# Kernel tuning notes

Measured on AMD Instinct MI355X. Metric: run time of the kernel, lower is better.

Reference implementation:

```python
import jax, jax.numpy as jnp
import numpy as np
import math

HIDDEN, N_HEADS = 128, 4
HEAD_DIM = HIDDEN // N_HEADS

def _silu(x):
    return x * jax.nn.sigmoid(x)

def _ln(x, g, b, eps=1e-5):
    m = jnp.mean(x, axis=-1, keepdims=True)
    v = jnp.mean((x - m) ** 2, axis=-1, keepdims=True)
    return (x - m) / jnp.sqrt(v + eps) * g + b


def setup_inputs() -> dict:
    key = jax.random.key(0)
    B, N, ND, ED, HD = 2, 512, 64, 32, 128
    ks = iter(jax.random.split(key, 64))
    def p(*shape):
        return jax.random.normal(next(ks), shape, jnp.float32) * 0.05
    d = {}
    d['h'] = jax.random.normal(next(ks), (B, N, ND), jnp.float32)
    d['x'] = jax.random.normal(next(ks), (B, N, 2), jnp.float32)
    d['e'] = jax.random.normal(next(ks), (B, N, N, ED), jnp.float32)
    msg_in = 2 * ND + ED + 1  # 161
    d['msg_W1'] = p(msg_in, HD); d['msg_b1'] = jnp.zeros((HD,), jnp.float32)
    d['msg_ln_g'] = jnp.ones((HD,), jnp.float32); d['msg_ln_b'] = jnp.zeros((HD,), jnp.float32)
    d['msg_W2'] = p(HD, HD); d['msg_b2'] = jnp.zeros((HD,), jnp.float32)
    d['msg_W3'] = p(HD, HD); d['msg_b3'] = jnp.zeros((HD,), jnp.float32)
    d['attn_W1'] = p(HD, HD // 2); d['attn_b1'] = jnp.zeros((HD // 2,), jnp.float32)
    d['attn_W2'] = p(HD // 2, N_HEADS); d['attn_b2'] = jnp.zeros((N_HEADS,), jnp.float32)
    d['val_W'] = p(HD, HD); d['val_b'] = jnp.zeros((HD,), jnp.float32)
    d['coord_W1'] = p(HD, HD // 2); d['coord_b1'] = jnp.zeros((HD // 2,), jnp.float32)
    d['coord_W2'] = p(HD // 2, 1)  # bias=False
    d['node_W1'] = p(ND + HD, HD); d['node_b1'] = jnp.zeros((HD,), jnp.float32)
    d['node_ln_g'] = jnp.ones((HD,), jnp.float32); d['node_ln_b'] = jnp.zeros((HD,), jnp.float32)
    d['node_W2'] = p(HD, ND); d['node_b2'] = jnp.zeros((ND,), jnp.float32)
    d['edge_W1'] = p(ED + HD, HD); d['edge_b1'] = jnp.zeros((HD,), jnp.float32)
    d['edge_ln_g'] = jnp.ones((HD,), jnp.float32); d['edge_ln_b'] = jnp.zeros((HD,), jnp.float32)
    d['edge_W2'] = p(HD, ED); d['edge_b2'] = jnp.zeros((ED,), jnp.float32)
    d['nn_g'] = jnp.ones((ND,), jnp.float32); d['nn_b'] = jnp.zeros((ND,), jnp.float32)
    d['en_g'] = jnp.ones((ED,), jnp.float32); d['en_b'] = jnp.zeros((ED,), jnp.float32)
    d['coord_scale'] = jnp.float32(0.1)
    return d


def reference(h, x, e,
              msg_W1, msg_b1, msg_ln_g, msg_ln_b, msg_W2, msg_b2, msg_W3, msg_b3,
              attn_W1, attn_b1, attn_W2, attn_b2, val_W, val_b,
              coord_W1, coord_b1, coord_W2,
              node_W1, node_b1, node_ln_g, node_ln_b, node_W2, node_b2,
              edge_W1, edge_b1, edge_ln_g, edge_ln_b, edge_W2, edge_b2,
              nn_g, nn_b, en_g, en_b, coord_scale):
    B, N, ND = h.shape
    # pairwise geometry: x_diff[b,i,j] = x[b,j] - x[b,i]
    x_diff = x[:, None, :, :] - x[:, :, None, :]           # (B,N,N,2)
    distances = jnp.linalg.norm(x_diff, axis=-1, keepdims=True)  # (B,N,N,1)
    h_i = jnp.broadcast_to(h[:, :, None, :], (B, N, N, ND))
    h_j = jnp.broadcast_to(h[:, None, :, :], (B, N, N, ND))
    msg_input = jnp.concatenate([h_i, h_j, e, distances], axis=-1)
    # message MLP (dropout is identity in eval)
    m = _silu(msg_input @ msg_W1 + msg_b1)
    m = _ln(m, msg_ln_g, msg_ln_b)
    m = _silu(m @ msg_W2 + msg_b2)
    messages = m @ msg_W3 + msg_b3                          # (B,N,N,HIDDEN)
    # attention over j (axis=2), multi-head
    attn_logits = (_silu(messages @ attn_W1 + attn_b1) @ attn_W2 + attn_b2)
    attn_logits = attn_logits / math.sqrt(HEAD_DIM)
    attn_weights = jax.nn.softmax(attn_logits, axis=2)      # (B,N,N,H)
    values = (messages @ val_W + val_b).reshape(B, N, N, N_HEADS, HEAD_DIM)
    messages_attended = jnp.einsum('bijh,bijhd->bihd', attn_weights, values)
    messages_attended = messages_attended.reshape(B, N, HIDDEN)
    # equivariant coordinate update
    coord_weights = _silu(messages @ coord_W1 + coord_b1) @ coord_W2  # (B,N,N,1)
    coord_weights = jnp.tanh(coord_weights / 10.0)
    x_diff_norm = x_diff / (distances + 1e-8)
    coord_update = jnp.sum(coord_weights * x_diff_norm, axis=2)      # (B,N,2)
    x_new = x + coord_scale * coord_update
    # node update
    h_input = jnp.concatenate([h, messages_attended], axis=-1)
    hh = _silu(h_input @ node_W1 + node_b1)
    hh = _ln(hh, node_ln_g, node_ln_b)
    hh = hh @ node_W2 + node_b2
    h_new = _ln(h + hh, nn_g, nn_b)
    # edge update
    e_input = jnp.concatenate([e, messages], axis=-1)
    ee = _silu(e_input @ edge_W1 + edge_b1)
    ee = _ln(ee, edge_ln_g, edge_ln_b)
    ee = ee @ edge_W2 + edge_b2
    e_new = _ln(e + ee, en_g, en_b)
    return (h_new, x_new, e_new)
```

## Files before the change

kernel.cpp:

```cpp
#include <hip/hip_runtime.h>
#include <math.h>

typedef __attribute__((ext_vector_type(8))) short short8;
typedef __attribute__((ext_vector_type(4))) short short4v;
typedef __attribute__((ext_vector_type(8))) unsigned short u16x8;
typedef __attribute__((ext_vector_type(4))) float f32x4;

#define NN 512
#define JT 32
#define STR 136
#define BUFSZ (JT * STR)
#define E2S 36

#define TOT_W 106496

__device__ __forceinline__ unsigned short f2b(float x) {
    return __builtin_bit_cast(unsigned short, (__bf16)x);
}
__device__ __forceinline__ float b2f(unsigned short v) {
    return __uint_as_float(((unsigned int)v) << 16);
}
__device__ __forceinline__ float silu_f(float v) { return v / (1.f + __expf(-v)); }

__device__ __forceinline__ float half_sum512(float v, float* s_red, int t) {
    if (t < 256) s_red[t] = v;
    __syncthreads();
    int tt = t & 127;
    for (int s = 64; s > 0; s >>= 1) {
        if (t < 256 && tt < s) s_red[t] += s_red[t + s];
        __syncthreads();
    }
    float r = (t < 256) ? s_red[t & 128] : 0.f;
    __syncthreads();
    return r;
}

__device__ __forceinline__ void frag_kf(int loc, int nK, int& k, int& f) {
    int jj = loc & 7;
    int lane = (loc >> 3) & 63;
    int fs = loc >> 9;
    int ks = fs % nK;
    int ft = fs / nK;
    k = ks * 32 + ((lane >> 4) << 3) + jj;
    f = ft * 16 + (lane & 15);
}

extern "C" __global__ void prepack_w(const float* __restrict__ msg_W1, const float* __restrict__ msg_W2,
                                     const float* __restrict__ msg_W3, const float* __restrict__ val_W,
                                     const float* __restrict__ attn_W1, const float* __restrict__ coord_W1,
                                     const float* __restrict__ edge_W1, const float* __restrict__ edge_W2,
                                     unsigned short* __restrict__ ws) {
    int idx = blockIdx.x * 256 + threadIdx.x;
    if (idx >= TOT_W) return;
    float v;
    int k, f;
    if (idx < 16384) {
        frag_kf(idx, 4, k, f);
        v = (k <= 96) ? msg_W1[(64 + k) * 128 + f] : 0.f;
    } else if (idx < 32768) {
        frag_kf(idx - 16384, 4, k, f);
        v = msg_W2[k * 128 + f];
    } else if (idx < 49152) {
        frag_kf(idx - 32768, 4, k, f);
        v = msg_W3[k * 128 + f];
    } else if (idx < 65536) {
        frag_kf(idx - 49152, 4, k, f);
        v = val_W[k * 128 + f];
    } else if (idx < 81920) {
        frag_kf(idx - 65536, 4, k, f);
        v = (f < 64) ? attn_W1[k * 64 + f] : coord_W1[k * 64 + (f - 64)];
    } else if (idx < 102400) {
        frag_kf(idx - 81920, 5, k, f);
        v = (k < 128) ? edge_W1[(32 + k) * 128 + f] : edge_W1[(k - 128) * 128 + f];
    } else {
        frag_kf(idx - 102400, 4, k, f);
        v = edge_W2[k * 32 + f];
    }
    ws[idx] = f2b(v);
}

struct Frag1 { f32x4 a[2]; };

__device__ __forceinline__ short8 wfrag(const unsigned short* base, int nK, int ft, int ks, int lane) {
    return *(const short8*)(base + (((ft * nK + ks) << 9) + (lane << 3)));
}

__device__ __forceinline__ void initF1(Frag1& F, const float* bias, int ft, int lane) {
    int q = lane >> 4;
    f32x4 bv = *(const f32x4*)(bias + ft * 16 + q * 4);
    F.a[0] = bv; F.a[1] = bv;
}

__device__ __forceinline__ void ldb(const unsigned short* B, int kcol, int lane, short8& b0, short8& b1) {
    int q8 = ((lane >> 4) << 3), l15 = lane & 15;
    b0 = *(const short8*)(B + l15 * STR + kcol + q8);
    b1 = *(const short8*)(B + (16 + l15) * STR + kcol + q8);
}

__device__ __forceinline__ void mfma2(Frag1& F, short8 a, short8 b0, short8 b1) {
    F.a[0] = __builtin_amdgcn_mfma_f32_16x16x32_bf16(a, b0, F.a[0], 0, 0, 0);
    F.a[1] = __builtin_amdgcn_mfma_f32_16x16x32_bf16(a, b1, F.a[1], 0, 0, 0);
}

__device__ __forceinline__ void storeF1(const Frag1& F, unsigned short* dbuf, int ft, int lane, int act) {
    int q = lane >> 4, l15 = lane & 15;
#pragma unroll
    for (int ji = 0; ji < 2; ji++) {
        int j = ji * 16 + l15;
        int f0 = ft * 16 + q * 4;
        f32x4 v = F.a[ji];
        short4v p;
#pragma unroll
        for (int r = 0; r < 4; r++) {
            float o = act ? silu_f(v[r]) : v[r];
            p[r] = (short)f2b(o);
        }
        *(short4v*)(dbuf + j * STR + f0) = p;
    }
}

__device__ __forceinline__ void ln_tile(unsigned short* buf, const float* g, const float* bv, int tt) {
    int j = tt >> 3, sub = tt & 7;
    unsigned short* p = buf + j * STR + sub * 16;
    u16x8 r0 = *(u16x8*)p;
    u16x8 r1 = *(u16x8*)(p + 8);
    float v[16];
#pragma unroll
    for (int i = 0; i < 8; i++) { v[i] = b2f(r0[i]); v[8 + i] = b2f(r1[i]); }
    float sm = 0.f;
#pragma unroll
    for (int i = 0; i < 16; i++) sm += v[i];
    sm += __shfl_xor(sm, 1); sm += __shfl_xor(sm, 2); sm += __shfl_xor(sm, 4);
    float mean = sm * 0.0078125f;
    float sq = 0.f;
#pragma unroll
    for (int i = 0; i < 16; i++) { float d = v[i] - mean; sq += d * d; }
    sq += __shfl_xor(sq, 1); sq += __shfl_xor(sq, 2); sq += __shfl_xor(sq, 4);
    float rstd = rsqrtf(sq * 0.0078125f + 1e-5f);
    u16x8 o0, o1;
#pragma unroll
    for (int i = 0; i < 8; i++) {
        o0[i] = f2b((v[i] - mean) * rstd * g[sub * 16 + i] + bv[sub * 16 + i]);
        o1[i] = f2b((v[8 + i] - mean) * rstd * g[sub * 16 + 8 + i] + bv[sub * 16 + 8 + i]);
    }
    *(u16x8*)p = o0;
    *(u16x8*)(p + 8) = o1;
}

extern "C" __global__ __launch_bounds__(512, 4)
void egnn_mfma(const float* __restrict__ h, const float* __restrict__ x, const float* __restrict__ e,
               const float* __restrict__ msg_W1, const float* __restrict__ msg_b1,
               const float* __restrict__ msg_ln_g, const float* __restrict__ msg_ln_b,
               const float* __restrict__ msg_b2, const float* __restrict__ msg_b3,
               const float* __restrict__ attn_b1, const float* __restrict__ attn_W2,
               const float* __restrict__ attn_b2, const float* __restrict__ val_b,
               const float* __restrict__ coord_b1, const float* __restrict__ coord_W2,
               const float* __restrict__ node_W1, const float* __restrict__ node_b1,
               const float* __restrict__ node_ln_g, const float* __restrict__ node_ln_b,
               const float* __restrict__ node_W2, const float* __restrict__ node_b2,
               const float* __restrict__ edge_b1, const float* __restrict__ edge_ln_g,
               const float* __restrict__ edge_ln_b, const float* __restrict__ edge_b2,
               const float* __restrict__ nn_g, const float* __restrict__ nn_b,
               const float* __restrict__ en_g, const float* __restrict__ en_b,
               const float* __restrict__ coord_scale_p,
               const unsigned short* __restrict__ wpk,
               float* __restrict__ out_h, float* __restrict__ out_x, float* __restrict__ out_e) {
    const int t = threadIdx.x;
    const int wave = t >> 6, lane = t & 63;
    const int biA = blockIdx.x * 2;
    const int biB = biA + 1;
    const int b = biA >> 9;

    __shared__ __align__(16) unsigned short smA[3 * BUFSZ];
    __shared__ __align__(16) unsigned short smB[3 * BUFSZ];
    unsigned short* B0a = smA;
    unsigned short* B1a = smA + BUFSZ;
    unsigned short* B2a = smA + 2 * BUFSZ;
    unsigned short* B0b = smB;
    unsigned short* B1b = smB + BUFSZ;
    unsigned short* B2b = smB + 2 * BUFSZ;
    __shared__ __align__(16) unsigned short s_e2a[32 * E2S];
    __shared__ __align__(16) unsigned short s_e2b[32 * E2S];

    __shared__ __align__(16) float s_bias1a[128], s_bias1b[128];
    __shared__ __align__(16) float s_b2c[128], s_b3c[128], s_bv[128], s_bac[128], s_be1[128];
    __shared__ __align__(16) float s_be2[32];
    __shared__ __align__(16) float s_mg[128], s_mb[128], s_eg[128], s_eb[128];
    __shared__ __align__(16) float s_cw2[64], s_aw2[4][64], s_ab2[4], s_eng[32], s_enb[32];
    __shared__ __align__(16) float s_lg[2][JT][4];
    __shared__ __align__(16) float s_hiA[64], s_hiB[64];

    const unsigned short* wG1 = wpk;
    const unsigned short* wG2 = wpk + 16384;
    const unsigned short* wG3 = wpk + 32768;
    const unsigned short* wV  = wpk + 49152;
    const unsigned short* wAC = wpk + 65536;
    const unsigned short* wE1 = wpk + 81920;
    const unsigned short* wE2 = wpk + 102400;

    if (t < 64) s_hiA[t] = h[(size_t)biA * 64 + t];
    else if (t < 128) s_hiB[t - 64] = h[(size_t)biB * 64 + (t - 64)];
    if (t < 128) {
        s_b2c[t] = msg_b2[t]; s_b3c[t] = msg_b3[t]; s_bv[t] = val_b[t];
        s_bac[t] = (t < 64) ? attn_b1[t] : coord_b1[t - 64];
        s_be1[t] = edge_b1[t];
        s_mg[t] = msg_ln_g[t]; s_mb[t] = msg_ln_b[t];
        s_eg[t] = edge_ln_g[t]; s_eb[t] = edge_ln_b[t];
    }
    if (t < 32) { s_be2[t] = edge_b2[t]; s_eng[t] = en_g[t]; s_enb[t] = en_b[t]; }
    if (t < 64) s_cw2[t] = coord_W2[t];
    if (t < 256) { int hh = t >> 6, k = t & 63; s_aw2[hh][k] = attn_W2[k * 4 + hh]; }
    if (t < 4) s_ab2[t] = attn_b2[t];
    __syncthreads();
    if (t < 256) {
        int ii = t >> 7, tt = t & 127;
        const float* hi = ii ? s_hiB : s_hiA;
        float acc = msg_b1[tt];
        for (int k = 0; k < 64; k++) acc = fmaf(hi[k], msg_W1[k * 128 + tt], acc);
        (ii ? s_bias1b : s_bias1a)[tt] = acc;
    }
    const float xiA0 = x[(size_t)biA * 2 + 0];
    const float xiA1 = x[(size_t)biA * 2 + 1];
    const float xiB0 = x[(size_t)biB * 2 + 0];
    const float xiB1 = x[(size_t)biB * 2 + 1];

    float m_run = -3e38f, l_run = 0.f, acc_run = 0.f;
    float cu_x = 0.f, cu_y = 0.f, xdn_x = 0.f, xdn_y = 0.f;

    const int l15 = lane & 15;

#pragma unroll 1
    for (int j0 = 0; j0 < NN; j0 += JT) {
        {
            int half = t >> 8, tt = t & 255;
            int j = tt >> 3, sub = tt & 7;
            int jj = j0 + j;
            if (half == 0) {
                const float* hp = h + ((size_t)(b * NN + jj)) * 64 + sub * 8;
                float4 h0 = *(const float4*)hp;
                float4 h1 = *(const float4*)(hp + 4);
                u16x8 o;
                o[0] = f2b(h0.x); o[1] = f2b(h0.y); o[2] = f2b(h0.z); o[3] = f2b(h0.w);
                o[4] = f2b(h1.x); o[5] = f2b(h1.y); o[6] = f2b(h1.z); o[7] = f2b(h1.w);
                *(u16x8*)(B0a + j * STR + sub * 8) = o;
                u16x8 z = (u16x8)0;
                if (sub > 4)       *(u16x8*)(B0a + j * STR + 96 + (sub - 4) * 8) = z;
                else if (sub >= 1) *(u16x8*)(B0b + j * STR + 96 + sub * 8) = z;
            } else {
                if (sub < 4) {
                    const f32x4* ea = (const f32x4*)(e + ((size_t)biA * NN + jj) * 32 + sub * 8);
                    f32x4 e0 = __builtin_nontemporal_load(ea);
                    f32x4 e1 = __builtin_nontemporal_load(ea + 1);
                    u16x8 oe;
                    oe[0] = f2b(e0[0]); oe[1] = f2b(e0[1]); oe[2] = f2b(e0[2]); oe[3] = f2b(e0[3]);
                    oe[4] = f2b(e1[0]); oe[5] = f2b(e1[1]); oe[6] = f2b(e1[2]); oe[7] = f2b(e1[3]);
                    *(u16x8*)(B0a + j * STR + 64 + sub * 8) = oe;
                } else {
                    const f32x4* eb = (const f32x4*)(e + ((size_t)biB * NN + jj) * 32 + (sub - 4) * 8);
                    f32x4 e0 = __builtin_nontemporal_load(eb);
                    f32x4 e1 = __builtin_nontemporal_load(eb + 1);
                    u16x8 oe;
                    oe[0] = f2b(e0[0]); oe[1] = f2b(e0[1]); oe[2] = f2b(e0[2]); oe[3] = f2b(e0[3]);
                    oe[4] = f2b(e1[0]); oe[5] = f2b(e1[1]); oe[6] = f2b(e1[2]); oe[7] = f2b(e1[3]);
                    *(u16x8*)(B0b + j * STR + 64 + (sub - 4) * 8) = oe;
                }
            }
        }
        if (t < JT) {
            int jj = j0 + t;
            float dx = x[(size_t)(b * NN + jj) * 2 + 0] - xiA0;
            float dy = x[(size_t)(b * NN + jj) * 2 + 1] - xiA1;
            float dist = sqrtf(dx * dx + dy * dy);
            float inv = 1.f / (dist + 1e-8f);
            xdn_x = dx * inv; xdn_y = dy * inv;
            u16x8 z = (u16x8)0;
            z[0] = f2b(dist);
            *(u16x8*)(B0a + t * STR + 96) = z;
        } else if (t >= 128 && t < 128 + JT) {
            int tb = t - 128;
            int jj = j0 + tb;
            float dx = x[(size_t)(b * NN + jj) * 2 + 0] - xiB0;
            float dy = x[(size_t)(b * NN + jj) * 2 + 1] - xiB1;
            float dist = sqrtf(dx * dx + dy * dy);
            float inv = 1.f / (dist + 1e-8f);
            xdn_x = dx * inv; xdn_y = dy * inv;
            u16x8 z = (u16x8)0;
            z[0] = f2b(dist);
            *(u16x8*)(B0b + tb * STR + 96) = z;
        }
        __syncthreads();

        {
            Frag1 Fa, Fb;
            initF1(Fa, s_bias1a, wave, lane);
            initF1(Fb, s_bias1b, wave, lane);
#pragma unroll
            for (int ks = 0; ks < 4; ks++) {
                short8 a = wfrag(wG1, 4, wave, ks, lane);
                short8 b0, b1;
                ldb(B0a, ks * 32, lane, b0, b1);
                mfma2(Fa, a, b0, b1);
                if (ks >= 2) ldb(B0b, ks * 32, lane, b0, b1);
                mfma2(Fb, a, b0, b1);
            }
            storeF1(Fa, B1a, wave, lane, 1);
            storeF1(Fb, B1b, wave, lane, 1);
        }
        __syncthreads();
        if (t < 256) ln_tile(B1a, s_mg, s_mb, t);
        else         ln_tile(B1b, s_mg, s_mb, t - 256);
        __syncthreads();

        {
            Frag1 Fa, Fb;
            initF1(Fa, s_b2c, wave, lane);
            initF1(Fb, s_b2c, wave, lane);
#pragma unroll
            for (int ks = 0; ks < 4; ks++) {
                short8 a = wfrag(wG2, 4, wave, ks, lane);
                short8 b0, b1;
                ldb(B1a, ks * 32, lane, b0, b1); mfma2(Fa, a, b0, b1);
                ldb(B1b, ks * 32, lane, b0, b1); mfma2(Fb, a, b0, b1);
            }
            storeF1(Fa, B2a, wave, lane, 1);
            storeF1(Fb, B2b, wave, lane, 1);
        }
        __syncthreads();

        {
            Frag1 Fa, Fb;
            initF1(Fa, s_b3c, wave, lane);
            initF1(Fb, s_b3c, wave, lane);
#pragma unroll
            for (int ks = 0; ks < 4; ks++) {
                short8 a = wfrag(wG3, 4, wave, ks, lane);
                short8 b0, b1;
                ldb(B2a, ks * 32, lane, b0, b1); mfma2(Fa, a, b0, b1);
                ldb(B2b, ks * 32, lane, b0, b1); mfma2(Fb, a, b0, b1);
            }
            storeF1(Fa, B1a, wave, lane, 0);
            storeF1(Fb, B1b, wave, lane, 0);
        }
        __syncthreads();

        {
            Frag1 FEa, FEb;
            initF1(FEa, s_be1, wave, lane);
            initF1(FEb, s_be1, wave, lane);
            {
                short8 a = wfrag(wE1, 5, wave, 4, lane);
                short8 b0, b1;
                ldb(B0a, 64, lane, b0, b1); mfma2(FEa, a, b0, b1);
                ldb(B0b, 64, lane, b0, b1); mfma2(FEb, a, b0, b1);
            }
            Frag1 FVa, FVb, FAa, FAb;
            initF1(FVa, s_bv, wave, lane);
            initF1(FVb, s_bv, wave, lane);
            initF1(FAa, s_bac, wave, lane);
            initF1(FAb, s_bac, wave, lane);
#pragma unroll
            for (int ks = 0; ks < 4; ks++) {
                short8 av = wfrag(wV, 4, wave, ks, lane);
                short8 aa = wfrag(wAC, 4, wave, ks, lane);
                short8 ae = wfrag(wE1, 5, wave, ks, lane);
                short8 b0, b1;
                ldb(B1a, ks * 32, lane, b0, b1);
                mfma2(FVa, av, b0, b1); mfma2(FAa, aa, b0, b1); mfma2(FEa, ae, b0, b1);
                ldb(B1b, ks * 32, lane, b0, b1);
                mfma2(FVb, av, b0, b1); mfma2(FAb, aa, b0, b1); mfma2(FEb, ae, b0, b1);
            }
            storeF1(FVa, B2a, wave, lane, 0);
            storeF1(FVb, B2b, wave, lane, 0);
            __syncthreads();
            storeF1(FAa, B0a, wave, lane, 1);
            storeF1(FAb, B0b, wave, lane, 1);
            storeF1(FEa, B1a, wave, lane, 1);
            storeF1(FEb, B1b, wave, lane, 1);
        }
        __syncthreads();

        if (t < 256) {
            ln_tile(B1a, s_eg, s_eb, t);
        } else {
            ln_tile(B1b, s_eg, s_eb, t - 256);
            int m = t - 256;
            int ii = m >> 7, mm = m & 127;
            const unsigned short* B0x = ii ? B0b : B0a;
            int j = mm >> 2, hh = mm & 3;
            float acc = s_ab2[hh];
#pragma unroll
            for (int m8 = 0; m8 < 8; m8++) {
                u16x8 r = *(u16x8*)(B0x + j * STR + m8 * 8);
#pragma unroll
                for (int i = 0; i < 8; i++) acc = fmaf(b2f(r[i]), s_aw2[hh][m8 * 8 + i], acc);
            }
            s_lg[ii][j][hh] = acc * 0.17677669529663687f;
        }
        __syncthreads();

        const int ii9 = t >> 8, tt9 = t & 255;
        const int j9 = tt9 >> 3, sub9 = tt9 & 7;
        f32x4 ev = __builtin_nontemporal_load(
            (const f32x4*)(e + ((size_t)(biA + ii9) * NN + (j0 + j9)) * 32 + sub9 * 4));

        if (wave < 4) {
            int ii = t >> 7, tt = t & 127;
            const unsigned short* B2x = ii ? B2b : B2a;
            int hh = tt >> 5;
#pragma unroll 4
            for (int j = 0; j < JT; j++) {
                float lg = s_lg[ii][j][hh];
                float nm = fmaxf(m_run, lg);
                float sc = __expf(m_run - nm);
                float p = __expf(lg - nm);
                float v = b2f(B2x[j * STR + tt]);
                acc_run = acc_run * sc + p * v;
                l_run = l_run * sc + p;
                m_run = nm;
            }
            if (tt < 32) {
                const unsigned short* B0x = ii ? B0b : B0a;
                float acc = 0.f;
#pragma unroll
                for (int m = 0; m < 8; m++) {
                    u16x8 r = *(u16x8*)(B0x + tt * STR + 64 + m * 8);
#pragma unroll
                    for (int i = 0; i < 8; i++) acc = fmaf(b2f(r[i]), s_cw2[m * 8 + i], acc);
                }
                float cw = tanhf(acc * 0.1f);
                cu_x = fmaf(cw, xdn_x, cu_x);
                cu_y = fmaf(cw, xdn_y, cu_y);
            }
        } else {
            int w4 = wave - 4, ih = w4 >> 1, wv = w4 & 1;
            const unsigned short* B1x = ih ? B1b : B1a;
            unsigned short* e2x = ih ? s_e2b : s_e2a;
            int q = lane >> 4;
            f32x4 bb = *(const f32x4*)(s_be2 + wv * 16 + q * 4);
            f32x4 a0 = bb, a1 = bb;
#pragma unroll
            for (int ks = 0; ks < 4; ks++) {
                short8 b0, b1;
                ldb(B1x, ks * 32, lane, b0, b1);
                short8 aw = wfrag(wE2, 4, wv, ks, lane);
                a0 = __builtin_amdgcn_mfma_f32_16x16x32_bf16(aw, b0, a0, 0, 0, 0);
                a1 = __builtin_amdgcn_mfma_f32_16x16x32_bf16(aw, b1, a1, 0, 0, 0);
            }
#pragma unroll
            for (int ji = 0; ji < 2; ji++) {
                int j = ji * 16 + l15;
                int f0 = wv * 16 + q * 4;
                f32x4 v = ji ? a1 : a0;
                short4v p;
#pragma unroll
                for (int r = 0; r < 4; r++) p[r] = (short)f2b(v[r]);
                *(short4v*)(e2x + j * E2S + f0) = p;
            }
        }
        __syncthreads();

        {
            const unsigned short* e2x = ii9 ? s_e2b : s_e2a;
            const unsigned short* p = e2x + j9 * E2S + sub9 * 4;
            float v0 = ev[0] + b2f(p[0]);
            float v1 = ev[1] + b2f(p[1]);
            float v2 = ev[2] + b2f(p[2]);
            float v3 = ev[3] + b2f(p[3]);
            float s = v0 + v1 + v2 + v3;
            s += __shfl_xor(s, 1); s += __shfl_xor(s, 2); s += __shfl_xor(s, 4);
            float mean = s * 0.03125f;
            float d0 = v0 - mean, d1 = v1 - mean, d2 = v2 - mean, d3 = v3 - mean;
            float sq = d0 * d0 + d1 * d1 + d2 * d2 + d3 * d3;
            sq += __shfl_xor(sq, 1); sq += __shfl_xor(sq, 2); sq += __shfl_xor(sq, 4);
            float rstd = rsqrtf(sq * 0.03125f + 1e-5f);
            f32x4 o;
            o[0] = d0 * rstd * s_eng[sub9 * 4 + 0] + s_enb[sub9 * 4 + 0];
            o[1] = d1 * rstd * s_eng[sub9 * 4 + 1] + s_enb[sub9 * 4 + 1];
            o[2] = d2 * rstd * s_eng[sub9 * 4 + 2] + s_enb[sub9 * 4 + 2];
            o[3] = d3 * rstd * s_eng[sub9 * 4 + 3] + s_enb[sub9 * 4 + 3];
            __builtin_nontemporal_store(o,
                (f32x4*)(out_e + ((size_t)(biA + ii9) * NN + (j0 + j9)) * 32 + sub9 * 4));
        }
    }

    float* s_ep = (float*)smA;
    float* s_hinA = s_ep;
    float* s_hinB = s_ep + 192;
    float* s_nhA  = s_ep + 384;
    float* s_nhB  = s_ep + 512;
    float* s_red  = s_ep + 640;

    __syncthreads();
    if (t < 256) {
        int ii = t >> 7, tt = t & 127;
        (ii ? s_hinB : s_hinA)[64 + tt] = acc_run / l_run;
    }
    if (t < 64) s_hinA[t] = s_hiA[t];
    else if (t < 128) s_hinB[t - 64] = s_hiB[t - 64];
    __syncthreads();

    if (t < 256) {
        int ii = t >> 7, tt = t & 127;
        const float* hin = ii ? s_hinB : s_hinA;
        float acc = node_b1[tt];
        for (int k4 = 0; k4 < 48; k4++) {
            f32x4 iv = *(const f32x4*)&hin[k4 * 4];
            acc = fmaf(iv[0], node_W1[(k4 * 4 + 0) * 128 + tt], acc);
            acc = fmaf(iv[1], node_W1[(k4 * 4 + 1) * 128 + tt], acc);
            acc = fmaf(iv[2], node_W1[(k4 * 4 + 2) * 128 + tt], acc);
            acc = fmaf(iv[3], node_W1[(k4 * 4 + 3) * 128 + tt], acc);
        }
        (ii ? s_nhB : s_nhA)[tt] = silu_f(acc);
    }
    __syncthreads();
    {
        int ii = t >> 7, tt = t & 127;
        float v = (t < 256) ? (ii ? s_nhB : s_nhA)[tt] : 0.f;
        float mean = half_sum512(v, s_red, t) * 0.0078125f;
        float d = (t < 256) ? (v - mean) : 0.f;
        float var = half_sum512(d * d, s_red, t) * 0.0078125f;
        float rstd = rsqrtf(var + 1e-5f);
        if (t < 256) (ii ? s_nhB : s_nhA)[tt] = d * rstd * node_ln_g[tt] + node_ln_b[tt];
    }
    __syncthreads();
    {
        int ii = t >> 7, tt = t & 127;
        float hv = 0.f;
        if (t < 256 && tt < 64) {
            const float* nh = ii ? s_nhB : s_nhA;
            float acc = node_b2[tt];
            for (int k4 = 0; k4 < 32; k4++) {
                f32x4 iv = *(const f32x4*)&nh[k4 * 4];
                acc = fmaf(iv[0], node_W2[(k4 * 4 + 0) * 64 + tt], acc);
                acc = fmaf(iv[1], node_W2[(k4 * 4 + 1) * 64 + tt], acc);
                acc = fmaf(iv[2], node_W2[(k4 * 4 + 2) * 64 + tt], acc);
                acc = fmaf(iv[3], node_W2[(k4 * 4 + 3) * 64 + tt], acc);
            }
            hv = acc + (ii ? s_hiB : s_hiA)[tt];
        }
        float mean = half_sum512((t < 256 && tt < 64) ? hv : 0.f, s_red, t) * 0.015625f;
        float d = (t < 256 && tt < 64) ? (hv - mean) : 0.f;
        float var = half_sum512(d * d, s_red, t) * 0.015625f;
        float rstd = rsqrtf(var + 1e-5f);
        if (t < 256 && tt < 64) out_h[(size_t)(biA + ii) * 64 + tt] = d * rstd * nn_g[tt] + nn_b[tt];
    }

    if (t < 256) {
        int tt = t & 127;
        if (tt < 32) {
            cu_x += __shfl_xor(cu_x, 16); cu_x += __shfl_xor(cu_x, 8);
            cu_x += __shfl_xor(cu_x, 4);  cu_x += __shfl_xor(cu_x, 2); cu_x += __shfl_xor(cu_x, 1);
            cu_y += __shfl_xor(cu_y, 16); cu_y += __shfl_xor(cu_y, 8);
            cu_y += __shfl_xor(cu_y, 4);  cu_y += __shfl_xor(cu_y, 2); cu_y += __shfl_xor(cu_y, 1);
            if (tt == 0) {
                float scl = coord_scale_p[0];
                if (t < 32) {
                    out_x[(size_t)biA * 2 + 0] = xiA0 + scl * cu_x;
                    out_x[(size_t)biA * 2 + 1] = xiA1 + scl * cu_y;
                } else {
                    out_x[(size_t)biB * 2 + 0] = xiB0 + scl * cu_x;
                    out_x[(size_t)biB * 2 + 1] = xiB1 + scl * cu_y;
                }
            }
        }
    }
}

extern "C" void kernel_launch(void* const* d_in, const int* in_sizes, int n_in,
                              void* d_out, int out_size, void* d_ws, size_t ws_size,
                              hipStream_t stream) {
    const float* h        = (const float*)d_in[0];
    const float* x        = (const float*)d_in[1];
    const float* e        = (const float*)d_in[2];
    const float* msg_W1   = (const float*)d_in[3];
    const float* msg_b1   = (const float*)d_in[4];
    const float* msg_ln_g = (const float*)d_in[5];
    const float* msg_ln_b = (const float*)d_in[6];
    const float* msg_W2   = (const float*)d_in[7];
    const float* msg_b2   = (const float*)d_in[8];
    const float* msg_W3   = (const float*)d_in[9];
    const float* msg_b3   = (const float*)d_in[10];
    const float* attn_W1  = (const float*)d_in[11];
    const float* attn_b1  = (const float*)d_in[12];
    const float* attn_W2  = (const float*)d_in[13];
    const float* attn_b2  = (const float*)d_in[14];
    const float* val_W    = (const float*)d_in[15];
    const float* val_b    = (const float*)d_in[16];
    const float* coord_W1 = (const float*)d_in[17];
    const float* coord_b1 = (const float*)d_in[18];
    const float* coord_W2 = (const float*)d_in[19];
    const float* node_W1  = (const float*)d_in[20];
    const float* node_b1  = (const float*)d_in[21];
    const float* node_ln_g= (const float*)d_in[22];
    const float* node_ln_b= (const float*)d_in[23];
    const float* node_W2  = (const float*)d_in[24];
    const float* node_b2  = (const float*)d_in[25];
    const float* edge_W1  = (const float*)d_in[26];
    const float* edge_b1  = (const float*)d_in[27];
    const float* edge_ln_g= (const float*)d_in[28];
    const float* edge_ln_b= (const float*)d_in[29];
    const float* edge_W2  = (const float*)d_in[30];
    const float* edge_b2  = (const float*)d_in[31];
    const float* nn_g     = (const float*)d_in[32];
    const float* nn_b     = (const float*)d_in[33];
    const float* en_g     = (const float*)d_in[34];
    const float* en_b     = (const float*)d_in[35];
    const float* coord_scale = (const float*)d_in[36];

    unsigned short* wpk = (unsigned short*)d_ws;

    float* out = (float*)d_out;
    float* out_h = out;
    float* out_x = out + (size_t)2 * 512 * 64;
    float* out_e = out_x + (size_t)2 * 512 * 2;

    hipLaunchKernelGGL(prepack_w, dim3((TOT_W + 255) / 256), dim3(256), 0, stream,
                       msg_W1, msg_W2, msg_W3, val_W, attn_W1, coord_W1, edge_W1, edge_W2, wpk);

    hipLaunchKernelGGL(egnn_mfma, dim3(512), dim3(512), 0, stream,
                       h, x, e,
                       msg_W1, msg_b1, msg_ln_g, msg_ln_b, msg_b2, msg_b3,
                       attn_b1, attn_W2, attn_b2, val_b, coord_b1, coord_W2,
                       node_W1, node_b1, node_ln_g, node_ln_b, node_W2, node_b2,
                       edge_b1, edge_ln_g, edge_ln_b, edge_b2,
                       nn_g, nn_b, en_g, en_b, coord_scale,
                       wpk, out_h, out_x, out_e);
}
```

Baseline: 643.0 us.

## Parallelize online softmax across lanes and rebalance edge-LN work across waves

Replaces the serial per-tile online-softmax loop (32 sequential exp/max updates per thread) with a lane-parallel version. Each lane computes one logit's probability, and warp shuffles produce the tile max and sum. The weighted-value accumulation moves to after the barrier and becomes a plain FMA loop over stored probabilities. The edge residual+LayerNorm epilogue and the e loads move entirely to waves 4-7, which handle both rows, so waves 0-3 only do attention and coord work. This rebalances the per-tile critical path, at the cost of an extra shared-memory round trip for probabilities and scale factors, plus an extra barrier at the end.

```diff
diff --git a/kernel.cpp b/kernel.cpp
--- a/kernel.cpp
+++ b/kernel.cpp
@@ -188,6 +188,7 @@
     __shared__ __align__(16) float s_mg[128], s_mb[128], s_eg[128], s_eb[128];
     __shared__ __align__(16) float s_cw2[64], s_aw2[4][64], s_ab2[4], s_eng[32], s_enb[32];
     __shared__ __align__(16) float s_lg[2][JT][4];
+    __shared__ __align__(16) float s_sc[2][4];
     __shared__ __align__(16) float s_hiA[64], s_hiB[64];
 
     const unsigned short* wG1 = wpk;
@@ -398,26 +399,39 @@
         }
         __syncthreads();
 
-        const int ii9 = t >> 8, tt9 = t & 255;
-        const int j9 = tt9 >> 3, sub9 = tt9 & 7;
-        f32x4 ev = __builtin_nontemporal_load(
-            (const f32x4*)(e + ((size_t)(biA + ii9) * NN + (j0 + j9)) * 32 + sub9 * 4));
-
-        if (wave < 4) {
+        f32x4 ev0, ev1;
+        if (t >= 256) {
+            int te = t - 256;
+            int j9 = te >> 3, sub9 = te & 7;
+            ev0 = __builtin_nontemporal_load(
+                (const f32x4*)(e + ((size_t)biA * NN + (j0 + j9)) * 32 + sub9 * 4));
+            ev1 = __builtin_nontemporal_load(
+                (const f32x4*)(e + ((size_t)biB * NN + (j0 + j9)) * 32 + sub9 * 4));
+        }
+
+        if (t < 256) {
             int ii = t >> 7, tt = t & 127;
-            const unsigned short* B2x = ii ? B2b : B2a;
-            int hh = tt >> 5;
-#pragma unroll 4
-            for (int j = 0; j < JT; j++) {
-                float lg = s_lg[ii][j][hh];
-                float nm = fmaxf(m_run, lg);
-                float sc = __expf(m_run - nm);
-                float p = __expf(lg - nm);
-                float v = b2f(B2x[j * STR + tt]);
-                acc_run = acc_run * sc + p * v;
-                l_run = l_run * sc + p;
-                m_run = nm;
-            }
+            int hh = tt >> 5, jj5 = tt & 31;
+            float lg = s_lg[ii][jj5][hh];
+            float gm = lg;
+            gm = fmaxf(gm, __shfl_xor(gm, 1));
+            gm = fmaxf(gm, __shfl_xor(gm, 2));
+            gm = fmaxf(gm, __shfl_xor(gm, 4));
+            gm = fmaxf(gm, __shfl_xor(gm, 8));
+            gm = fmaxf(gm, __shfl_xor(gm, 16));
+            float nm = fmaxf(m_run, gm);
+            float sc = __expf(m_run - nm);
+            float p = __expf(lg - nm);
+            float ps = p;
+            ps += __shfl_xor(ps, 1);
+            ps += __shfl_xor(ps, 2);
+            ps += __shfl_xor(ps, 4);
+            ps += __shfl_xor(ps, 8);
+            ps += __shfl_xor(ps, 16);
+            l_run = l_run * sc + ps;
+            m_run = nm;
+            s_lg[ii][jj5][hh] = p;
+            if (jj5 == 0) s_sc[ii][hh] = sc;
             if (tt < 32) {
                 const unsigned short* B0x = ii ? B0b : B0a;
                 float acc = 0.f;
@@ -459,27 +473,44 @@
         }
         __syncthreads();
 
-        {
-            const unsigned short* e2x = ii9 ? s_e2b : s_e2a;
-            const unsigned short* p = e2x + j9 * E2S + sub9 * 4;
-            float v0 = ev[0] + b2f(p[0]);
-            float v1 = ev[1] + b2f(p[1]);
-            float v2 = ev[2] + b2f(p[2]);
-            float v3 = ev[3] + b2f(p[3]);
-            float s = v0 + v1 + v2 + v3;
-            s += __shfl_xor(s, 1); s += __shfl_xor(s, 2); s += __shfl_xor(s, 4);
-            float mean = s * 0.03125f;
-            float d0 = v0 - mean, d1 = v1 - mean, d2 = v2 - mean, d3 = v3 - mean;
-            float sq = d0 * d0 + d1 * d1 + d2 * d2 + d3 * d3;
-            sq += __shfl_xor(sq, 1); sq += __shfl_xor(sq, 2); sq += __shfl_xor(sq, 4);
-            float rstd = rsqrtf(sq * 0.03125f + 1e-5f);
-            f32x4 o;
-            o[0] = d0 * rstd * s_eng[sub9 * 4 + 0] + s_enb[sub9 * 4 + 0];
-            o[1] = d1 * rstd * s_eng[sub9 * 4 + 1] + s_enb[sub9 * 4 + 1];
-            o[2] = d2 * rstd * s_eng[sub9 * 4 + 2] + s_enb[sub9 * 4 + 2];
-            o[3] = d3 * rstd * s_eng[sub9 * 4 + 3] + s_enb[sub9 * 4 + 3];
-            __builtin_nontemporal_store(o,
-                (f32x4*)(out_e + ((size_t)(biA + ii9) * NN + (j0 + j9)) * 32 + sub9 * 4));
+        if (t < 256) {
+            int ii = t >> 7, f = t & 127;
+            int hh = f >> 5;
+            const unsigned short* B2x = ii ? B2b : B2a;
+            const float* pp = &s_lg[ii][0][hh];
+            float accl = acc_run * s_sc[ii][hh];
+#pragma unroll 8
+            for (int j = 0; j < JT; j++)
+                accl = fmaf(pp[j * 4], b2f(B2x[j * STR + f]), accl);
+            acc_run = accl;
+        } else {
+            int te = t - 256;
+            int j9 = te >> 3, sub9 = te & 7;
+#pragma unroll
+            for (int ii = 0; ii < 2; ii++) {
+                const unsigned short* e2x = ii ? s_e2b : s_e2a;
+                f32x4 ev = ii ? ev1 : ev0;
+                int biX = biA + ii;
+                const unsigned short* p = e2x + j9 * E2S + sub9 * 4;
+                float v0 = ev[0] + b2f(p[0]);
+                float v1 = ev[1] + b2f(p[1]);
+                float v2 = ev[2] + b2f(p[2]);
+                float v3 = ev[3] + b2f(p[3]);
+                float s = v0 + v1 + v2 + v3;
+                s += __shfl_xor(s, 1); s += __shfl_xor(s, 2); s += __shfl_xor(s, 4);
+                float mean = s * 0.03125f;
+                float d0 = v0 - mean, d1 = v1 - mean, d2 = v2 - mean, d3 = v3 - mean;
+                float sq = d0 * d0 + d1 * d1 + d2 * d2 + d3 * d3;
+                sq += __shfl_xor(sq, 1); sq += __shfl_xor(sq, 2); sq += __shfl_xor(sq, 4);
+                float rstd = rsqrtf(sq * 0.03125f + 1e-5f);
+                f32x4 o;
+                o[0] = d0 * rstd * s_eng[sub9 * 4 + 0] + s_enb[sub9 * 4 + 0];
+                o[1] = d1 * rstd * s_eng[sub9 * 4 + 1] + s_enb[sub9 * 4 + 1];
+                o[2] = d2 * rstd * s_eng[sub9 * 4 + 2] + s_enb[sub9 * 4 + 2];
+                o[3] = d3 * rstd * s_eng[sub9 * 4 + 3] + s_enb[sub9 * 4 + 3];
+                __builtin_nontemporal_store(o,
+                    (f32x4*)(out_e + ((size_t)biX * NN + (j0 + j9)) * 32 + sub9 * 4));
+            }
         }
     }
 
@@ -491,9 +522,11 @@
     float* s_red  = s_ep + 640;
 
     __syncthreads();
+    if (t < 256 && (t & 31) == 0) s_sc[t >> 7][(t >> 5) & 3] = l_run;
+    __syncthreads();
     if (t < 256) {
         int ii = t >> 7, tt = t & 127;
-        (ii ? s_hinB : s_hinA)[64 + tt] = acc_run / l_run;
+        (ii ? s_hinB : s_hinA)[64 + tt] = acc_run / s_sc[ii][tt >> 5];
     }
     if (t < 64) s_hinA[t] = s_hiA[t];
     else if (t < 128) s_hinB[t - 64] = s_hiB[t - 64];
```

Result: slower. 660.3 us (+2.7%).
